# Kernel optimization log

Hardware: AMD Instinct MI355X
Metric: run time of the kernel (lower is better)

## Reference

```python
import jax, jax.numpy as jnp
import numpy as np


def setup_inputs() -> dict:
    key = jax.random.key(0)
    ks = jax.random.split(key, 8)
    B, N, D, H = 8, 512, 64, 64
    user_embeddings = jax.random.normal(ks[0], (B, N, D), dtype=jnp.float32)
    past_lengths = jax.random.randint(ks[1], (B,), 0, N)
    valid_mask = jnp.ones((B, N), dtype=jnp.float32)
    # MLP params: Linear(4D -> H), PReLU (single slope), Linear(H -> 1)
    s1 = 1.0 / np.sqrt(4 * D)
    s2 = 1.0 / np.sqrt(H)
    W1 = jax.random.uniform(ks[2], (H, 4 * D), minval=-s1, maxval=s1, dtype=jnp.float32)
    b1 = jax.random.uniform(ks[3], (H,), minval=-s1, maxval=s1, dtype=jnp.float32)
    prelu_a = jnp.float32(0.25)
    W2 = jax.random.uniform(ks[4], (1, H), minval=-s2, maxval=s2, dtype=jnp.float32)
    b2 = jax.random.uniform(ks[5], (1,), minval=-s2, maxval=s2, dtype=jnp.float32)
    return {"past_lengths": past_lengths, "user_embeddings": user_embeddings,
            "valid_mask": valid_mask, "W1": W1, "b1": b1, "prelu_a": prelu_a,
            "W2": W2, "b2": b2}


def reference(past_lengths, user_embeddings, valid_mask, W1, b1, prelu_a, W2, b2):
    # DIN local activation attention with causal mask.
    # Original math: h = W1 @ concat(Q, K, Q-K, Q*K) + b1 per (q,k) pair.
    # Split W1 into its 4 D-sized blocks so the concat tensor [B,N,N,4D] is
    # never materialized; the pairwise hidden [B,N,N,H] is the only big buffer.
    B, N, D = user_embeddings.shape
    Wq, Wk, Wd, Wm = jnp.split(W1, 4, axis=1)  # each [H, D]
    x = user_embeddings
    # Q and (Q-K)'s +Q part -> per-query term; K and (Q-K)'s -K part -> per-key term
    hq = jnp.einsum('bqd,hd->bqh', x, Wq + Wd)          # [B,N,H]
    hk = jnp.einsum('bkd,hd->bkh', x, Wk - Wd)          # [B,N,H]
    hm = jnp.einsum('bqd,bkd,hd->bqkh', x, x, Wm)       # [B,N,N,H] (Q*K term)
    h = hq[:, :, None, :] + hk[:, None, :, :] + hm + b1
    h = jnp.where(h > 0, h, prelu_a * h)                # PReLU
    scores = jnp.einsum('bqkh,h->bqk', h, W2[0]) + b2[0]  # [B,N,N]
    causal = jnp.tril(jnp.ones((N, N), dtype=scores.dtype))
    scores = scores * causal[None, :, :]
    scores = scores * valid_mask[:, None, :]            # key-side padding mask
    encoded = jnp.einsum('bqk,bkd->bqd', scores, x)     # weighted sum (no softmax)
    return encoded
```

## Files before the change

kernel.cpp:

```cpp
#include <hip/hip_runtime.h>

#define NB 8
#define NN 512

#define WS_WMF 0
#define WS_HQ  4096
#define WS_BF  266240
#define WS_XE  528384

typedef float fx4 __attribute__((ext_vector_type(4)));
typedef short sx8 __attribute__((ext_vector_type(8)));
typedef int   ix4 __attribute__((ext_vector_type(4)));

static __device__ inline unsigned short f2bf(float f) {
    unsigned u = __float_as_uint(f);
    return (unsigned short)((u + 0x7FFFu + ((u >> 16) & 1u)) >> 16);
}

__global__ __launch_bounds__(256) void prep(const float* __restrict__ x,
                                            const float* __restrict__ vm,
                                            const float* __restrict__ W1,
                                            const float* __restrict__ b1,
                                            float* __restrict__ ws) {
    __shared__ float lwq[64 * 65];
    __shared__ float lwk[64 * 65];
    __shared__ float xs[256];
    const int t = threadIdx.x;
    const int blk = blockIdx.x;

    {
        int d = t & 63, hb = t >> 6;
        #pragma unroll 4
        for (int i = 0; i < 16; ++i) {
            int h = i * 4 + hb;
            float a = W1[h * 256 + d];
            float bb = W1[h * 256 + 64 + d];
            float c = W1[h * 256 + 128 + d];
            lwq[d * 65 + h] = a + c;
            lwk[d * 65 + h] = bb - c;
        }
    }
    const int r0 = blk * 4;
    xs[t] = x[r0 * 64 + t];
    __syncthreads();

    {
        int r = t >> 6, h = t & 63;
        const float* xr = xs + r * 64;
        float aq = b1[h], ak = 0.f;
        #pragma unroll
        for (int dd = 0; dd < 64; ++dd) {
            float xv = xr[dd];
            aq = fmaf(xv, lwq[dd * 65 + h], aq);
            ak = fmaf(xv, lwk[dd * 65 + h], ak);
        }
        int row = r0 + r;
        (ws + WS_HQ)[row * 64 + h] = aq;
        unsigned short* bfp = (unsigned short*)(ws + WS_BF);
        int bb = row >> 9, k = row & 511;
        int tt = k >> 4, nn = k & 15;
        int c = 2 + (h >> 5);
        int qd = (h >> 3) & 3, j = h & 7;
        int ln = qd * 16 + nn;
        bfp[((((bb * 32 + tt) * 4 + c) * 64 + ln) << 3) + j] = f2bf(ak);
    }

    if (blk < 256) {
        int b = blk >> 5, t5 = blk & 31;
        if (t < 128) {
            unsigned short* bfp = (unsigned short*)(ws + WS_BF);
            int c = t >> 6, L = t & 63;
            int nn = L & 15, qd = L >> 4;
            const float* src = x + ((b * 512 + t5 * 16 + nn) * 64 + c * 32 + qd * 8);
            fx4 v0 = *(const fx4*)src;
            fx4 v1 = *(const fx4*)(src + 4);
            uint4 o;
            o.x = (unsigned)f2bf(v0[0]) | ((unsigned)f2bf(v0[1]) << 16);
            o.y = (unsigned)f2bf(v0[2]) | ((unsigned)f2bf(v0[3]) << 16);
            o.z = (unsigned)f2bf(v1[0]) | ((unsigned)f2bf(v1[1]) << 16);
            o.w = (unsigned)f2bf(v1[2]) | ((unsigned)f2bf(v1[3]) << 16);
            *(uint4*)(bfp + ((((b * 32 + t5) * 4 + c) * 64 + L) << 3)) = o;
        }
        {
            unsigned short* xep = (unsigned short*)(ws + WS_XE);
            int c32 = t5 >> 1, half = t5 & 1;
            int nt = t >> 6, r = t & 63;
            int L = half * 32 + (r & 31);
            int j0 = (r >> 5) * 4;
            int quad = L >> 4, nn = L & 15;
            unsigned short u[4];
            #pragma unroll
            for (int i = 0; i < 4; ++i) {
                int key = c32 * 32 + quad * 8 + j0 + i;
                float v = x[(b * 512 + key) * 64 + nt * 16 + nn] * vm[b * 512 + key];
                u[i] = f2bf(v);
            }
            uint2 o;
            o.x = (unsigned)u[0] | ((unsigned)u[1] << 16);
            o.y = (unsigned)u[2] | ((unsigned)u[3] << 16);
            *(uint2*)(xep + (((((b * 16 + c32) * 4 + nt) * 64 + L) << 3) + j0)) = o;
        }
    } else if (blk < 258) {
        float* wmf = ws + WS_WMF;
        int e = (blk - 256) * 256 + t;
        int slot = e >> 6, lane = e & 63;
        int ht = slot >> 1, hf = slot & 1;
        int m = lane & 15, qd = lane >> 4;
        int h = ht * 16 + m;
        int dbase = hf * 32 + qd * 8;
        #pragma unroll
        for (int j = 0; j < 8; ++j)
            wmf[e * 8 + j] = W1[h * 256 + 192 + dbase + j];
    }
}

__global__ __launch_bounds__(512, 2) void k2_main(const float* __restrict__ x,
                                                  const float* __restrict__ prelu_a,
                                                  const float* __restrict__ W2,
                                                  const float* __restrict__ b2,
                                                  const float* __restrict__ ws,
                                                  float* __restrict__ out) {
    const int tid  = threadIdx.x;
    const int lane = tid & 63;
    const int w    = tid >> 6;
    const int blk  = blockIdx.x;
    const int b    = blk >> 6;
    const int j    = blk & 63;
    const int q    = (w < 4) ? (4 * j + w) : (508 - 4 * j + (w - 4));
    const int n    = lane & 15, quad = lane >> 4;
    const int bq   = b * 512 + q;
    const int cmaxw = q >> 5;
    const int cblk  = (511 - 4 * j) >> 5;

    const float* wmf = ws + WS_WMF;
    const float* hq  = ws + WS_HQ;
    const unsigned short* bfp = (const unsigned short*)(ws + WS_BF);
    const unsigned short* xep = (const unsigned short*)(ws + WS_XE);

    const float pa  = prelu_a[0];
    const float b2v = b2[0];

    __shared__ uint4 bufS[2][512];
    __shared__ uint4 bufE[2][256];

    float hqr[4][4], w2r[4][4];
    #pragma unroll
    for (int ht = 0; ht < 4; ++ht) {
        fx4 vh = *(const fx4*)(hq + bq * 64 + ht * 16 + quad * 4);
        fx4 vw = *(const fx4*)(W2 + ht * 16 + quad * 4);
        #pragma unroll
        for (int r = 0; r < 4; ++r) { hqr[ht][r] = vh[r]; w2r[ht][r] = vw[r]; }
    }

    float xq[2][8];
    {
        const float* xp = x + bq * 64 + quad * 8;
        fx4 t0 = *(const fx4*)xp;
        fx4 t1 = *(const fx4*)(xp + 4);
        fx4 t2 = *(const fx4*)(xp + 32);
        fx4 t3 = *(const fx4*)(xp + 36);
        #pragma unroll
        for (int jj = 0; jj < 4; ++jj) {
            xq[0][jj] = t0[jj]; xq[0][4 + jj] = t1[jj];
            xq[1][jj] = t2[jj]; xq[1][4 + jj] = t3[jj];
        }
    }

    sx8 afrag[4][2];
    #pragma unroll
    for (int ht = 0; ht < 4; ++ht)
        #pragma unroll
        for (int hf = 0; hf < 2; ++hf) {
            const float* wp = wmf + (((ht * 2 + hf) * 64 + lane) << 3);
            fx4 w0 = *(const fx4*)wp;
            fx4 w1 = *(const fx4*)(wp + 4);
            sx8 a;
            #pragma unroll
            for (int jj = 0; jj < 4; ++jj) {
                a[jj]     = (short)f2bf(w0[jj] * xq[hf][jj]);
                a[4 + jj] = (short)f2bf(w1[jj] * xq[hf][4 + jj]);
            }
            afrag[ht][hf] = a;
        }

    sx8 oh[4];
    #pragma unroll
    for (int ht = 0; ht < 4; ++ht) {
        sx8 a;
        #pragma unroll
        for (int jj = 0; jj < 8; ++jj) {
            int hp = (ht >> 1) * 32 + quad * 8 + jj;
            a[jj] = (hp == ht * 16 + n) ? (short)0x3F80 : (short)0;
        }
        oh[ht] = a;
    }

    int idxs[8];
    #pragma unroll
    for (int jj = 0; jj < 8; ++jj) idxs[jj] = ((quad * 8 + jj) & 15) << 2;
    const unsigned sel = (quad < 2) ? 0x05040100u : 0x07060302u;

    fx4 eacc[4];
    #pragma unroll
    for (int nt = 0; nt < 4; ++nt) eacc[nt] = (fx4){0.f, 0.f, 0.f, 0.f};

    {
        const uint4* s = (const uint4*)(bfp + (unsigned)(b * 32) * 2048);
        bufS[0][tid] = s[tid];
        if (tid < 256) {
            const uint4* s2 = (const uint4*)(xep + (unsigned)(b * 16) * 2048);
            bufE[0][tid] = s2[tid];
        }
    }
    __syncthreads();

    for (int c = 0; c <= cblk; ++c) {
        uint4 st, st2;
        if (c < cblk) {
            int cc = c + 1;
            st = ((const uint4*)(bfp + (unsigned)(b * 32 + 2 * cc) * 2048))[tid];
            if (tid < 256)
                st2 = ((const uint4*)(xep + (unsigned)(b * 16 + cc) * 2048))[tid];
        }

        if (c <= cmaxw) {
            const unsigned short* ls = (const unsigned short*)&bufS[c & 1][0] + lane * 8;
            sx8 fa0 = *(const sx8*)(ls);
            sx8 fa1 = *(const sx8*)(ls + 512);
            sx8 fa2 = *(const sx8*)(ls + 1024);
            sx8 fa3 = *(const sx8*)(ls + 1536);
            sx8 fb0 = *(const sx8*)(ls + 2048);
            sx8 fb1 = *(const sx8*)(ls + 2560);
            sx8 fb2 = *(const sx8*)(ls + 3072);
            sx8 fb3 = *(const sx8*)(ls + 3584);

            fx4 accA[4], accB[4];
            #pragma unroll
            for (int ht = 0; ht < 4; ++ht) {
                accA[ht] = (fx4){hqr[ht][0], hqr[ht][1], hqr[ht][2], hqr[ht][3]};
                accB[ht] = accA[ht];
            }
            #pragma unroll
            for (int ht = 0; ht < 4; ++ht) {
                accA[ht] = __builtin_amdgcn_mfma_f32_16x16x32_bf16(afrag[ht][0], fa0, accA[ht], 0, 0, 0);
                accB[ht] = __builtin_amdgcn_mfma_f32_16x16x32_bf16(afrag[ht][0], fb0, accB[ht], 0, 0, 0);
            }
            #pragma unroll
            for (int ht = 0; ht < 4; ++ht) {
                accA[ht] = __builtin_amdgcn_mfma_f32_16x16x32_bf16(afrag[ht][1], fa1, accA[ht], 0, 0, 0);
                accB[ht] = __builtin_amdgcn_mfma_f32_16x16x32_bf16(afrag[ht][1], fb1, accB[ht], 0, 0, 0);
            }
            #pragma unroll
            for (int ht = 0; ht < 4; ++ht) {
                accA[ht] = __builtin_amdgcn_mfma_f32_16x16x32_bf16(oh[ht], (ht < 2) ? fa2 : fa3, accA[ht], 0, 0, 0);
                accB[ht] = __builtin_amdgcn_mfma_f32_16x16x32_bf16(oh[ht], (ht < 2) ? fb2 : fb3, accB[ht], 0, 0, 0);
            }

            float s0a = 0.f, s0b = 0.f, s1a = 0.f, s1b = 0.f;
            #pragma unroll
            for (int ht = 0; ht < 2; ++ht)
                #pragma unroll
                for (int r = 0; r < 4; ++r) {
                    float za = accA[ht][r], zb = accB[ht][r];
                    s0a = fmaf(w2r[ht][r], fmaxf(za, za * pa), s0a);
                    s1a = fmaf(w2r[ht][r], fmaxf(zb, zb * pa), s1a);
                }
            #pragma unroll
            for (int ht = 2; ht < 4; ++ht)
                #pragma unroll
                for (int r = 0; r < 4; ++r) {
                    float za = accA[ht][r], zb = accB[ht][r];
                    s0b = fmaf(w2r[ht][r], fmaxf(za, za * pa), s0b);
                    s1b = fmaf(w2r[ht][r], fmaxf(zb, zb * pa), s1b);
                }
            float s0 = s0a + s0b, s1 = s1a + s1b;
            s0 += __shfl_xor(s0, 16, 64);
            s0 += __shfl_xor(s0, 32, 64);
            s1 += __shfl_xor(s1, 16, 64);
            s1 += __shfl_xor(s1, 32, 64);
            int k0 = c * 32 + n;
            s0 = (k0 <= q)      ? s0 + b2v : 0.f;
            s1 = (k0 + 16 <= q) ? s1 + b2v : 0.f;

            unsigned packed = (unsigned)f2bf(s0) | ((unsigned)f2bf(s1) << 16);
            int g[8];
            #pragma unroll
            for (int jj = 0; jj < 8; ++jj)
                g[jj] = __builtin_amdgcn_ds_bpermute(idxs[jj], (int)packed);
            ix4 sw_;
            sw_[0] = (int)__builtin_amdgcn_perm((unsigned)g[1], (unsigned)g[0], sel);
            sw_[1] = (int)__builtin_amdgcn_perm((unsigned)g[3], (unsigned)g[2], sel);
            sw_[2] = (int)__builtin_amdgcn_perm((unsigned)g[5], (unsigned)g[4], sel);
            sw_[3] = (int)__builtin_amdgcn_perm((unsigned)g[7], (unsigned)g[6], sel);
            sx8 sfrag = __builtin_bit_cast(sx8, sw_);

            const unsigned short* le = (const unsigned short*)&bufE[c & 1][0] + lane * 8;
            sx8 e0 = *(const sx8*)(le);
            sx8 e1 = *(const sx8*)(le + 512);
            sx8 e2 = *(const sx8*)(le + 1024);
            sx8 e3 = *(const sx8*)(le + 1536);

            eacc[0] = __builtin_amdgcn_mfma_f32_16x16x32_bf16(sfrag, e0, eacc[0], 0, 0, 0);
            eacc[1] = __builtin_amdgcn_mfma_f32_16x16x32_bf16(sfrag, e1, eacc[1], 0, 0, 0);
            eacc[2] = __builtin_amdgcn_mfma_f32_16x16x32_bf16(sfrag, e2, eacc[2], 0, 0, 0);
            eacc[3] = __builtin_amdgcn_mfma_f32_16x16x32_bf16(sfrag, e3, eacc[3], 0, 0, 0);
        }

        if (c < cblk) {
            int cc = c + 1;
            bufS[cc & 1][tid] = st;
            if (tid < 256) bufE[cc & 1][tid] = st2;
        }
        __syncthreads();
    }

    float ov = eacc[0][0];
    if (quad == 1) ov = eacc[1][0];
    if (quad == 2) ov = eacc[2][0];
    if (quad == 3) ov = eacc[3][0];
    out[bq * 64 + lane] = ov;
}

extern "C" void kernel_launch(void* const* d_in, const int* in_sizes, int n_in,
                              void* d_out, int out_size, void* d_ws, size_t ws_size,
                              hipStream_t stream) {
    const float* x   = (const float*)d_in[1];
    const float* vmk = (const float*)d_in[2];
    const float* W1  = (const float*)d_in[3];
    const float* b1  = (const float*)d_in[4];
    const float* pa  = (const float*)d_in[5];
    const float* W2  = (const float*)d_in[6];
    const float* b2  = (const float*)d_in[7];
    float* ws  = (float*)d_ws;
    float* out = (float*)d_out;

    hipLaunchKernelGGL(prep, dim3(NB * NN / 4), dim3(256), 0, stream,
                       x, vmk, W1, b1, ws);
    hipLaunchKernelGGL(k2_main, dim3(NB * 64), dim3(512), 0, stream,
                       x, pa, W2, b2, ws, out);
}
```

Before: 108.8 us.

## Restructure causal work split into paired query bands with 4-wave blocks

```diff
diff --git a/kernel.cpp b/kernel.cpp
--- a/kernel.cpp
+++ b/kernel.cpp
@@ -114,7 +114,7 @@
     }
 }
 
-__global__ __launch_bounds__(512, 2) void k2_main(const float* __restrict__ x,
+__global__ __launch_bounds__(256, 2) void k2_main(const float* __restrict__ x,
                                                   const float* __restrict__ prelu_a,
                                                   const float* __restrict__ W2,
                                                   const float* __restrict__ b2,
@@ -125,12 +125,10 @@
     const int w    = tid >> 6;
     const int blk  = blockIdx.x;
     const int b    = blk >> 6;
-    const int j    = blk & 63;
-    const int q    = (w < 4) ? (4 * j + w) : (508 - 4 * j + (w - 4));
+    const int rest = blk & 63;
+    const int m    = rest >> 3;
+    const int s    = rest & 7;
     const int n    = lane & 15, quad = lane >> 4;
-    const int bq   = b * 512 + q;
-    const int cmaxw = q >> 5;
-    const int cblk  = (511 - 4 * j) >> 5;
 
     const float* wmf = ws + WS_WMF;
     const float* hq  = ws + WS_HQ;
@@ -142,47 +140,15 @@
 
     __shared__ uint4 bufS[2][512];
     __shared__ uint4 bufE[2][256];
-
-    float hqr[4][4], w2r[4][4];
+    __shared__ unsigned strip[4][16];
+
+    float w2r[4][4];
     #pragma unroll
     for (int ht = 0; ht < 4; ++ht) {
-        fx4 vh = *(const fx4*)(hq + bq * 64 + ht * 16 + quad * 4);
         fx4 vw = *(const fx4*)(W2 + ht * 16 + quad * 4);
         #pragma unroll
-        for (int r = 0; r < 4; ++r) { hqr[ht][r] = vh[r]; w2r[ht][r] = vw[r]; }
-    }
-
-    float xq[2][8];
-    {
-        const float* xp = x + bq * 64 + quad * 8;
-        fx4 t0 = *(const fx4*)xp;
-        fx4 t1 = *(const fx4*)(xp + 4);
-        fx4 t2 = *(const fx4*)(xp + 32);
-        fx4 t3 = *(const fx4*)(xp + 36);
-        #pragma unroll
-        for (int jj = 0; jj < 4; ++jj) {
-            xq[0][jj] = t0[jj]; xq[0][4 + jj] = t1[jj];
-            xq[1][jj] = t2[jj]; xq[1][4 + jj] = t3[jj];
-        }
-    }
-
-    sx8 afrag[4][2];
-    #pragma unroll
-    for (int ht = 0; ht < 4; ++ht)
-        #pragma unroll
-        for (int hf = 0; hf < 2; ++hf) {
-            const float* wp = wmf + (((ht * 2 + hf) * 64 + lane) << 3);
-            fx4 w0 = *(const fx4*)wp;
-            fx4 w1 = *(const fx4*)(wp + 4);
-            sx8 a;
-            #pragma unroll
-            for (int jj = 0; jj < 4; ++jj) {
-                a[jj]     = (short)f2bf(w0[jj] * xq[hf][jj]);
-                a[4 + jj] = (short)f2bf(w1[jj] * xq[hf][4 + jj]);
-            }
-            afrag[ht][hf] = a;
-        }
-
+        for (int r = 0; r < 4; ++r) w2r[ht][r] = vw[r];
+    }
     sx8 oh[4];
     #pragma unroll
     for (int ht = 0; ht < 4; ++ht) {
@@ -194,37 +160,76 @@
         }
         oh[ht] = a;
     }
-
-    int idxs[8];
-    #pragma unroll
-    for (int jj = 0; jj < 8; ++jj) idxs[jj] = ((quad * 8 + jj) & 15) << 2;
     const unsigned sel = (quad < 2) ? 0x05040100u : 0x07060302u;
 
-    fx4 eacc[4];
-    #pragma unroll
-    for (int nt = 0; nt < 4; ++nt) eacc[nt] = (fx4){0.f, 0.f, 0.f, 0.f};
-
     {
-        const uint4* s = (const uint4*)(bfp + (unsigned)(b * 32) * 2048);
-        bufS[0][tid] = s[tid];
-        if (tid < 256) {
-            const uint4* s2 = (const uint4*)(xep + (unsigned)(b * 16) * 2048);
-            bufE[0][tid] = s2[tid];
-        }
+        const uint4* srcS = (const uint4*)(bfp + (unsigned)(b * 32) * 2048);
+        bufS[0][tid]       = srcS[tid];
+        bufS[0][tid + 256] = srcS[tid + 256];
+        bufE[0][tid] = ((const uint4*)(xep + (unsigned)(b * 16) * 2048))[tid];
     }
     __syncthreads();
 
-    for (int c = 0; c <= cblk; ++c) {
-        uint4 st, st2;
-        if (c < cblk) {
-            int cc = c + 1;
-            st = ((const uint4*)(bfp + (unsigned)(b * 32 + 2 * cc) * 2048))[tid];
-            if (tid < 256)
-                st2 = ((const uint4*)(xep + (unsigned)(b * 16 + cc) * 2048))[tid];
-        }
-
-        if (c <= cmaxw) {
-            const unsigned short* ls = (const unsigned short*)&bufS[c & 1][0] + lane * 8;
+    int r = 0;
+    #pragma unroll 1
+    for (int ph = 0; ph < 2; ++ph) {
+        const int band = ph ? (15 - m) : m;
+        const int q    = band * 32 + s * 4 + w;
+        const int bq   = b * 512 + q;
+        const int cmax = band;
+
+        float hqr[4][4];
+        #pragma unroll
+        for (int ht = 0; ht < 4; ++ht) {
+            fx4 vh = *(const fx4*)(hq + bq * 64 + ht * 16 + quad * 4);
+            #pragma unroll
+            for (int rr = 0; rr < 4; ++rr) hqr[ht][rr] = vh[rr];
+        }
+        float xq[2][8];
+        {
+            const float* xp = x + bq * 64 + quad * 8;
+            fx4 t0 = *(const fx4*)xp;
+            fx4 t1 = *(const fx4*)(xp + 4);
+            fx4 t2 = *(const fx4*)(xp + 32);
+            fx4 t3 = *(const fx4*)(xp + 36);
+            #pragma unroll
+            for (int jj = 0; jj < 4; ++jj) {
+                xq[0][jj] = t0[jj]; xq[0][4 + jj] = t1[jj];
+                xq[1][jj] = t2[jj]; xq[1][4 + jj] = t3[jj];
+            }
+        }
+        sx8 afrag[4][2];
+        #pragma unroll
+        for (int ht = 0; ht < 4; ++ht)
+            #pragma unroll
+            for (int hf = 0; hf < 2; ++hf) {
+                const float* wp = wmf + (((ht * 2 + hf) * 64 + lane) << 3);
+                fx4 w0 = *(const fx4*)wp;
+                fx4 w1 = *(const fx4*)(wp + 4);
+                sx8 a;
+                #pragma unroll
+                for (int jj = 0; jj < 4; ++jj) {
+                    a[jj]     = (short)f2bf(w0[jj] * xq[hf][jj]);
+                    a[4 + jj] = (short)f2bf(w1[jj] * xq[hf][4 + jj]);
+                }
+                afrag[ht][hf] = a;
+            }
+
+        fx4 eacc[4];
+        #pragma unroll
+        for (int nt = 0; nt < 4; ++nt) eacc[nt] = (fx4){0.f, 0.f, 0.f, 0.f};
+
+        for (int c = 0; c <= cmax; ++c, ++r) {
+            uint4 st0, st1, stE;
+            if (r < 16) {
+                int nc = (r + 1 <= m) ? (r + 1) : (r - m);
+                const uint4* srcS = (const uint4*)(bfp + (unsigned)(b * 32 + 2 * nc) * 2048);
+                st0 = srcS[tid];
+                st1 = srcS[tid + 256];
+                stE = ((const uint4*)(xep + (unsigned)(b * 16 + nc) * 2048))[tid];
+            }
+
+            const unsigned short* ls = (const unsigned short*)&bufS[r & 1][0] + lane * 8;
             sx8 fa0 = *(const sx8*)(ls);
             sx8 fa1 = *(const sx8*)(ls + 512);
             sx8 fa2 = *(const sx8*)(ls + 1024);
@@ -260,18 +265,18 @@
             #pragma unroll
             for (int ht = 0; ht < 2; ++ht)
                 #pragma unroll
-                for (int r = 0; r < 4; ++r) {
-                    float za = accA[ht][r], zb = accB[ht][r];
-                    s0a = fmaf(w2r[ht][r], fmaxf(za, za * pa), s0a);
-                    s1a = fmaf(w2r[ht][r], fmaxf(zb, zb * pa), s1a);
+                for (int rr = 0; rr < 4; ++rr) {
+                    float za = accA[ht][rr], zb = accB[ht][rr];
+                    s0a = fmaf(w2r[ht][rr], fmaxf(za, za * pa), s0a);
+                    s1a = fmaf(w2r[ht][rr], fmaxf(zb, zb * pa), s1a);
                 }
             #pragma unroll
             for (int ht = 2; ht < 4; ++ht)
                 #pragma unroll
-                for (int r = 0; r < 4; ++r) {
-                    float za = accA[ht][r], zb = accB[ht][r];
-                    s0b = fmaf(w2r[ht][r], fmaxf(za, za * pa), s0b);
-                    s1b = fmaf(w2r[ht][r], fmaxf(zb, zb * pa), s1b);
+                for (int rr = 0; rr < 4; ++rr) {
+                    float za = accA[ht][rr], zb = accB[ht][rr];
+                    s0b = fmaf(w2r[ht][rr], fmaxf(za, za * pa), s0b);
+                    s1b = fmaf(w2r[ht][rr], fmaxf(zb, zb * pa), s1b);
                 }
             float s0 = s0a + s0b, s1 = s1a + s1b;
             s0 += __shfl_xor(s0, 16, 64);
@@ -283,18 +288,18 @@
             s1 = (k0 + 16 <= q) ? s1 + b2v : 0.f;
 
             unsigned packed = (unsigned)f2bf(s0) | ((unsigned)f2bf(s1) << 16);
-            int g[8];
-            #pragma unroll
-            for (int jj = 0; jj < 8; ++jj)
-                g[jj] = __builtin_amdgcn_ds_bpermute(idxs[jj], (int)packed);
+            if (quad == 0) strip[w][n] = packed;
+            const unsigned* sp = &strip[w][(quad & 1) * 8];
+            uint4 wv0 = *(const uint4*)sp;
+            uint4 wv1 = *(const uint4*)(sp + 4);
             ix4 sw_;
-            sw_[0] = (int)__builtin_amdgcn_perm((unsigned)g[1], (unsigned)g[0], sel);
-            sw_[1] = (int)__builtin_amdgcn_perm((unsigned)g[3], (unsigned)g[2], sel);
-            sw_[2] = (int)__builtin_amdgcn_perm((unsigned)g[5], (unsigned)g[4], sel);
-            sw_[3] = (int)__builtin_amdgcn_perm((unsigned)g[7], (unsigned)g[6], sel);
+            sw_[0] = (int)__builtin_amdgcn_perm(wv0.y, wv0.x, sel);
+            sw_[1] = (int)__builtin_amdgcn_perm(wv0.w, wv0.z, sel);
+            sw_[2] = (int)__builtin_amdgcn_perm(wv1.y, wv1.x, sel);
+            sw_[3] = (int)__builtin_amdgcn_perm(wv1.w, wv1.z, sel);
             sx8 sfrag = __builtin_bit_cast(sx8, sw_);
 
-            const unsigned short* le = (const unsigned short*)&bufE[c & 1][0] + lane * 8;
+            const unsigned short* le = (const unsigned short*)&bufE[r & 1][0] + lane * 8;
             sx8 e0 = *(const sx8*)(le);
             sx8 e1 = *(const sx8*)(le + 512);
             sx8 e2 = *(const sx8*)(le + 1024);
@@ -304,21 +309,21 @@
             eacc[1] = __builtin_amdgcn_mfma_f32_16x16x32_bf16(sfrag, e1, eacc[1], 0, 0, 0);
             eacc[2] = __builtin_amdgcn_mfma_f32_16x16x32_bf16(sfrag, e2, eacc[2], 0, 0, 0);
             eacc[3] = __builtin_amdgcn_mfma_f32_16x16x32_bf16(sfrag, e3, eacc[3], 0, 0, 0);
-        }
-
-        if (c < cblk) {
-            int cc = c + 1;
-            bufS[cc & 1][tid] = st;
-            if (tid < 256) bufE[cc & 1][tid] = st2;
-        }
-        __syncthreads();
-    }
-
-    float ov = eacc[0][0];
-    if (quad == 1) ov = eacc[1][0];
-    if (quad == 2) ov = eacc[2][0];
-    if (quad == 3) ov = eacc[3][0];
-    out[bq * 64 + lane] = ov;
+
+            if (r < 16) {
+                bufS[(r + 1) & 1][tid]       = st0;
+                bufS[(r + 1) & 1][tid + 256] = st1;
+                bufE[(r + 1) & 1][tid]       = stE;
+            }
+            __syncthreads();
+        }
+
+        float ov = eacc[0][0];
+        if (quad == 1) ov = eacc[1][0];
+        if (quad == 2) ov = eacc[2][0];
+        if (quad == 3) ov = eacc[3][0];
+        out[bq * 64 + lane] = ov;
+    }
 }
 
 extern "C" void kernel_launch(void* const* d_in, const int* in_sizes, int n_in,
@@ -336,6 +341,6 @@
 
     hipLaunchKernelGGL(prep, dim3(NB * NN / 4), dim3(256), 0, stream,
                        x, vmk, W1, b1, ws);
-    hipLaunchKernelGGL(k2_main, dim3(NB * 64), dim3(512), 0, stream,
+    hipLaunchKernelGGL(k2_main, dim3(NB * 64), dim3(256), 0, stream,
                        x, pa, W2, b2, ws, out);
 }
```

After: 103.1 us. 1.06x faster.
